# Kernel optimization log

Hardware: AMD Instinct MI355X
Metric: run time of the kernel (lower is better)

The kernel has to match this reference:

```python
import jax, jax.numpy as jnp
import numpy as np

EPS_BN = 1e-5
DIVERSITY_TEMP = 100.0  # lucidrains codebook_diversity_temperature default
COMMIT_W = 1.0
DIVERSITY_W = 1.0
ORTHO_W = 1.0


def conv1d(x, w, b=None, stride=1, pad=0):
    # x: [B,C,T], w: [O,I,K] (torch layout)
    y = jax.lax.conv_general_dilated(x, w, (stride,), [(pad, pad)],
                                     dimension_numbers=('NCH', 'OIH', 'NCH'))
    if b is not None:
        y = y + b[None, :, None]
    return y


def conv1d_transpose(x, w_torch, stride, pad):
    # torch ConvTranspose1d weight: (in, out, k). Equivalent input-dilated conv
    # with flipped kernel and padding k-1-pad.
    w = jnp.flip(jnp.transpose(w_torch, (1, 0, 2)), axis=2)  # -> (out,in,k)
    k = w.shape[2]
    p = k - 1 - pad
    return jax.lax.conv_general_dilated(x, w, (1,), [(p, p)],
                                        lhs_dilation=(stride,),
                                        dimension_numbers=('NCH', 'OIH', 'NCH'))


def batchnorm(x, g, b):
    # training-mode BatchNorm1d: stats over (batch, time) per channel
    m = x.mean(axis=(0, 2), keepdims=True)
    v = x.var(axis=(0, 2), keepdims=True)
    return (x - m) * jax.lax.rsqrt(v + EPS_BN) * g[None, :, None] + b[None, :, None]


def setup_inputs():
    key = jax.random.key(0)
    ks = jax.random.split(key, 10)
    f32 = jnp.float32
    rn = lambda k, shape, s: jax.random.normal(k, shape, f32) * s
    return {
        'x': jax.random.normal(ks[0], (8, 1, 24000), f32),
        # encoder: 1->16->32->64
        'w1': rn(ks[1], (16, 1, 5), 0.3), 'b1': jnp.zeros(16, f32),
        'g1': jnp.ones(16, f32), 'be1': jnp.zeros(16, f32),
        'w2': rn(ks[2], (32, 16, 5), 0.1), 'b2': jnp.zeros(32, f32),
        'g2': jnp.ones(32, f32), 'be2': jnp.zeros(32, f32),
        'w3': rn(ks[3], (64, 32, 25), 0.05), 'b3': jnp.zeros(64, f32),
        'g3': jnp.ones(64, f32), 'be3': jnp.zeros(64, f32),
        # VQ codebook [codebook_size=8192, dim=64]
        'embed': jax.random.normal(ks[4], (8192, 64), f32),
        # decoder
        'dw1': rn(ks[5], (64, 64, 25), 0.05),  # ConvTranspose1d weight (in,out,k)
        'dg1': jnp.ones(64, f32), 'dbe1': jnp.zeros(64, f32),
        'dw2': rn(ks[6], (64, 64, 5), 0.1), 'db2': jnp.zeros(64, f32),
        'dg2': jnp.ones(64, f32), 'dbe2': jnp.zeros(64, f32),
        'dw3': rn(ks[7], (1, 64, 1), 0.2), 'db3': jnp.zeros(1, f32),
        # fixed random subset for orthogonal reg (orthogonal_reg_max_codes=256)
        'ortho_idx': jax.random.randint(ks[8], (256,), 0, 8192),
    }


def reference(x, w1, b1, g1, be1, w2, b2, g2, be2, w3, b3, g3, be3,
              embed, dw1, dg1, dbe1, dw2, db2, dg2, dbe2, dw3, db3, ortho_idx):
    # ---- encoder ----
    h = batchnorm(jax.nn.silu(conv1d(x, w1, b1, 1, 2)), g1, be1)
    h = batchnorm(jax.nn.silu(conv1d(h, w2, b2, 1, 2)), g2, be2)
    z = batchnorm(jnp.tanh(conv1d(h, w3, b3, 12, 12)), g3, be3)  # [B,64,N]
    B, C, N = z.shape
    zf = jnp.transpose(z, (0, 2, 1)).reshape(B * N, C)  # [B*N, 64]

    # ---- VQ: nearest neighbor over codebook ----
    d2 = (jnp.sum(zf * zf, -1, keepdims=True) - 2.0 * (zf @ embed.T)
          + jnp.sum(embed * embed, -1)[None, :])          # [B*N, K]
    dist = jnp.sqrt(jnp.clip(d2, 1e-12))                  # euclidean (cdist p=2)
    idx = jnp.argmin(d2, axis=-1)                         # [B*N]
    q = embed[idx]                                        # codebook gather

    commit = jnp.mean((jax.lax.stop_gradient(q) - zf) ** 2)

    prob = jax.nn.softmax(-dist * DIVERSITY_TEMP, axis=-1)
    avg_prob = prob.mean(axis=0)                          # [K]
    diversity = jnp.sum(avg_prob * jnp.log(jnp.clip(avg_prob, 1e-30)))

    codes = embed[ortho_idx]                              # [256, 64]
    normed = codes * jax.lax.rsqrt(jnp.sum(codes * codes, -1, keepdims=True) + 1e-12)
    cos = normed @ normed.T
    n = codes.shape[0]
    ortho = jnp.sum(cos * cos) / (n * n) - 1.0 / n

    loss = COMMIT_W * commit + DIVERSITY_W * diversity + ORTHO_W * ortho

    # straight-through estimator
    q_st = zf + jax.lax.stop_gradient(q - zf)
    zq = jnp.transpose(q_st.reshape(B, N, C), (0, 2, 1))  # [B,64,N]

    # ---- decoder ----
    d = batchnorm(jax.nn.silu(conv1d_transpose(zq, dw1, 12, 12)), dg1, dbe1)
    d = batchnorm(jax.nn.silu(conv1d(d, dw2, db2, 1, 2)), dg2, dbe2)
    recon = conv1d(d, dw3, db3, 1, 0)

    T = x.shape[2]
    cur = recon.shape[2]
    if cur > T:
        recon = recon[:, :, :T]
    elif cur < T:
        recon = jnp.pad(recon, ((0, 0), (0, 0), (0, T - cur)))
    return recon, idx.reshape(B, N), loss, (commit, diversity, ortho)
```

## Files before the change

### kernel.cpp

```cpp
#include <hip/hip_runtime.h>
#include <math.h>
#include <float.h>

#define DEV __device__ __forceinline__

#define BB 8
#define TT 24000
#define TD 23989
#define NZ 2000
#define ROWS 16000
#define NE 8192
#define NCG 8

typedef __attribute__((ext_vector_type(8))) short bf16x8;
typedef __attribute__((ext_vector_type(4))) float f32x4;

__device__ double g_st[640];
__device__ double g_misc[2];
__device__ float  g_e2[NE];
__device__ float  g_avg[NE];
__device__ float  g_z2[ROWS];
__device__ float  g_rdm[ROWS];
__device__ int    g_rix[ROWS];
__device__ float  g_ob[256 * 64];
__device__ float  g_pmd[ROWS * NCG];
__device__ int    g_pmi[ROWS * NCG];
__device__ int    g_pcc[ROWS * NCG];
__device__ float2 g_cand[ROWS * 256];
__device__ unsigned short g_zbh[ROWS * 64], g_zbl[ROWS * 64];
__device__ unsigned short g_ebh[NE * 64],  g_ebl[NE * 64];
__device__ float  g_s1[16], g_sh1[16];
__device__ float  g_s2[32], g_sh2[32];
__device__ float  g_sd1[64], g_shd1[64];
__device__ float  g_w2f[2560];
__device__ float  g_b2f[32];
__device__ float  g_w3f[64 * 32 * 25];
__device__ float  g_b3f[64];
__device__ float  g_dw2f[64 * 5 * 64];
__device__ float  g_db2f[64];
__device__ float  g_dw1t[64 * 64 * 25];
__device__ float  g_zbn[ROWS * 64];
__device__ double g_zbnd[ROWS * 64];
__device__ float  g_zq[BB * 64 * NZ];
__device__ float  g_y1[BB * 16 * TT];
__device__ float  g_zpre[BB * 64 * NZ];
__device__ float  g_yd1[BB * 64 * TD];
__device__ float  g_y2[BB * 32 * TT];
__device__ float  g_yd2[BB * 64 * TD];

DEV float wsum(float v){
  #pragma unroll
  for (int o = 32; o; o >>= 1) v += __shfl_xor(v, o, 64);
  return v;
}
DEV int clampc(int c){ return c < 0 ? 0 : (c > NE - 1 ? NE - 1 : c); }
DEV float bss(unsigned short s){ union { unsigned u; float f; } v; v.u = ((unsigned)s) << 16; return v.f; }
DEV unsigned short f2bs(float f){
  union { float f; unsigned u; } v; v.f = f;
  unsigned r = (v.u + 0x7FFF + ((v.u >> 16) & 1)) >> 16;
  return (unsigned short)r;
}

__global__ void k_zero(){
  int i = blockIdx.x * 256 + threadIdx.x;
  if (i < 640) g_st[i] = 0.0;
  if (i < 2) g_misc[i] = 0.0;
  if (i < NE) g_avg[i] = 0.f;
}

__global__ void k_embprep(const float* __restrict__ embed){
  int gt = blockIdx.x * 256 + threadIdx.x;
  int gs = gridDim.x * 256;
  for (int i = gt; i < NE * 64; i += gs){
    float v = embed[i];
    unsigned short h = f2bs(v);
    g_ebh[i] = h;
    g_ebl[i] = f2bs(v - bss(h));
  }
  for (int c = gt; c < NE; c += gs){
    float s = 0.f;
    for (int j = 0; j < 64; j++){ float v = embed[c * 64 + j]; s += v * v; }
    g_e2[c] = s;
  }
}

__global__ void k_zsplit(){
  int i = blockIdx.x * 256 + threadIdx.x;
  if (i < ROWS * 64){
    float v = g_zbn[i];
    unsigned short h = f2bs(v);
    g_zbh[i] = h;
    g_zbl[i] = f2bs(v - bss(h));
  }
}

__global__ void k_conv1(const float* __restrict__ x, const float* __restrict__ w1,
                        const float* __restrict__ b1){
  int b = blockIdx.y, t0 = blockIdx.x * 256, tid = threadIdx.x;
  __shared__ float xs[260], wl[80], bl[16], sacc[16], qacc[16];
  if (tid < 80) wl[tid] = w1[tid];
  if (tid < 16){ bl[tid] = b1[tid]; sacc[tid] = 0.f; qacc[tid] = 0.f; }
  for (int i = tid; i < 260; i += 256){ int g = t0 - 2 + i; xs[i] = ((unsigned)g < TT) ? x[b * TT + g] : 0.f; }
  __syncthreads();
  int t = t0 + tid;
  bool ok = t < TT;
  float xv[5];
  #pragma unroll
  for (int k = 0; k < 5; k++) xv[k] = xs[tid + k];
  float out[16];
  #pragma unroll
  for (int c = 0; c < 16; c++){
    float a = bl[c];
    #pragma unroll
    for (int k = 0; k < 5; k++) a += wl[c * 5 + k] * xv[k];
    float o = ok ? a / (1.f + expf(-a)) : 0.f;
    out[c] = o;
    if (ok) g_y1[(b * 16 + c) * TT + t] = o;
  }
  int lane = tid & 63;
  #pragma unroll
  for (int c = 0; c < 16; c++){
    float s = wsum(out[c]);
    float q = wsum(out[c] * out[c]);
    if (lane == 0){ atomicAdd(&sacc[c], s); atomicAdd(&qacc[c], q); }
  }
  __syncthreads();
  if (tid < 16){ atomicAdd(&g_st[tid * 2], (double)sacc[tid]); atomicAdd(&g_st[tid * 2 + 1], (double)qacc[tid]); }
}

__global__ void k_fold2(const float* __restrict__ g1, const float* __restrict__ be1,
                        const float* __restrict__ w2, const float* __restrict__ b2){
  int tid = threadIdx.x;
  if (blockIdx.x == 0 && tid < 16){
    double m = g_st[tid * 2] / 192000.0, v = g_st[tid * 2 + 1] / 192000.0 - m * m;
    float s = g1[tid] / sqrtf((float)v + 1e-5f);
    g_s1[tid] = s; g_sh1[tid] = be1[tid] - (float)m * s;
  }
  if (blockIdx.x == 0 && tid < 32) g_b2f[tid] = b2[tid];
  int gt = blockIdx.x * 256 + tid;
  for (int i = gt; i < 2560; i += 8 * 256){
    int co = i & 31, r = i >> 5, k = r % 5, ci = r / 5;
    g_w2f[i] = w2[(co * 16 + ci) * 5 + k];
  }
}

__global__ void __launch_bounds__(256) k_conv2(){
  int b = blockIdx.y, t0 = blockIdx.x * 256, tid = threadIdx.x;
  __shared__ float xs[16][260];
  __shared__ float sacc[32], qacc[32];
  __shared__ float s1l[16], sh1l[16];
  int lane = tid & 63, wv = tid >> 6;
  int cb = wv * 8;
  if (tid < 32){ sacc[tid] = 0.f; qacc[tid] = 0.f; }
  if (tid < 16){ s1l[tid] = g_s1[tid]; sh1l[tid] = g_sh1[tid]; }
  __syncthreads();
  for (int i = tid; i < 16 * 260; i += 256){
    int ci = i / 260, tt = i - ci * 260, g = t0 - 2 + tt;
    xs[ci][tt] = ((unsigned)g < TT) ? (s1l[ci] * g_y1[(b * 16 + ci) * TT + g] + sh1l[ci]) : 0.f;
  }
  __syncthreads();
  float acc[4][8];
  #pragma unroll
  for (int j = 0; j < 4; j++)
    #pragma unroll
    for (int i = 0; i < 8; i++) acc[j][i] = g_b2f[cb + i];
  for (int ci = 0; ci < 16; ci++){
    #pragma unroll
    for (int k = 0; k < 5; k++){
      const float4* wp = (const float4*)(g_w2f + (ci * 5 + k) * 32 + cb);
      float4 w0 = wp[0], w1v = wp[1];
      float wr[8] = { w0.x, w0.y, w0.z, w0.w, w1v.x, w1v.y, w1v.z, w1v.w };
      #pragma unroll
      for (int j = 0; j < 4; j++){
        float xv = xs[ci][lane + 64 * j + k];
        #pragma unroll
        for (int i = 0; i < 8; i++) acc[j][i] += wr[i] * xv;
      }
    }
  }
  #pragma unroll
  for (int i = 0; i < 8; i++){
    int co = cb + i;
    float s = 0.f, q = 0.f;
    #pragma unroll
    for (int j = 0; j < 4; j++){
      int t = t0 + lane + 64 * j;
      bool ok = t < TT;
      float a = acc[j][i];
      float o = ok ? a / (1.f + expf(-a)) : 0.f;
      if (ok) g_y2[(b * 32 + co) * TT + t] = o;
      s += o; q += o * o;
    }
    s = wsum(s); q = wsum(q);
    if (lane == 0){ atomicAdd(&sacc[co], s); atomicAdd(&qacc[co], q); }
  }
  __syncthreads();
  if (tid < 32){ atomicAdd(&g_st[128 + tid * 2], (double)sacc[tid]); atomicAdd(&g_st[128 + tid * 2 + 1], (double)qacc[tid]); }
}

__global__ void k_fold3(const float* __restrict__ g2, const float* __restrict__ be2,
                        const float* __restrict__ w3, const float* __restrict__ b3){
  int tid = threadIdx.x;
  if (blockIdx.x == 0 && tid < 32){
    double m = g_st[128 + tid * 2] / 192000.0, v = g_st[128 + tid * 2 + 1] / 192000.0 - m * m;
    float s = g2[tid] / sqrtf((float)v + 1e-5f);
    g_s2[tid] = s; g_sh2[tid] = be2[tid] - (float)m * s;
  }
  if (blockIdx.x == 0 && tid >= 64 && tid < 128) g_b3f[tid - 64] = b3[tid - 64];
  int gt = blockIdx.x * 256 + tid;
  for (int i = gt; i < 64 * 32 * 25; i += 64 * 256){
    int co = i & 63, r = i >> 6, k = r % 25, ci = r / 25;
    g_w3f[i] = w3[(co * 32 + ci) * 25 + k];
  }
}

__global__ void __launch_bounds__(256) k_conv3(){
  __shared__ float xs[32][400];
  __shared__ float s2l[32], sh2l[32];
  int tid = threadIdx.x, b = blockIdx.y, t0 = blockIdx.x * 32;
  int lane = tid & 63, wv = tid >> 6;
  int cb = wv * 16;
  int tl = lane & 31, h = lane >> 5;
  if (tid < 32){ s2l[tid] = g_s2[tid]; sh2l[tid] = g_sh2[tid]; }
  __syncthreads();
  int p0 = t0 * 12 - 12;
  for (int i = tid; i < 32 * 397; i += 256){
    int ci = i / 397, pp = i - ci * 397, g = p0 + pp;
    xs[ci][pp] = ((unsigned)g < TT) ? (s2l[ci] * g_y2[(b * 32 + ci) * TT + g] + sh2l[ci]) : 0.f;
  }
  __syncthreads();
  float acc[16];
  #pragma unroll
  for (int i = 0; i < 16; i++) acc[i] = 0.f;
  for (int cii = 0; cii < 16; cii++){
    int ci = h * 16 + cii;
    #pragma unroll
    for (int k = 0; k < 25; k++){
      float xv = xs[ci][tl * 12 + k];
      const float4* wp = (const float4*)(g_w3f + (ci * 25 + k) * 64 + cb);
      float4 a0 = wp[0], a1 = wp[1], a2 = wp[2], a3 = wp[3];
      acc[0] += a0.x * xv; acc[1] += a0.y * xv; acc[2] += a0.z * xv; acc[3] += a0.w * xv;
      acc[4] += a1.x * xv; acc[5] += a1.y * xv; acc[6] += a1.z * xv; acc[7] += a1.w * xv;
      acc[8] += a2.x * xv; acc[9] += a2.y * xv; acc[10] += a2.z * xv; acc[11] += a2.w * xv;
      acc[12] += a3.x * xv; acc[13] += a3.y * xv; acc[14] += a3.z * xv; acc[15] += a3.w * xv;
    }
  }
  #pragma unroll
  for (int i = 0; i < 16; i++) acc[i] += __shfl_xor(acc[i], 32, 64);
  int t = t0 + tl;
  if (h == 0 && t < NZ){
    #pragma unroll
    for (int i = 0; i < 16; i++)
      g_zpre[(b * 64 + cb + i) * NZ + t] = tanhf(acc[i] + g_b3f[cb + i]);
  }
}

__global__ void k_stats(int which, int L, int stoff){
  const float* p = (which == 0) ? g_zpre : (which == 1) ? g_yd1 : g_yd2;
  int co = blockIdx.y, t0 = blockIdx.x * 256, tid = threadIdx.x;
  int t = t0 + tid;
  float s = 0.f, q = 0.f;
  if (t < L){
    for (int b = 0; b < BB; b++){ float v = p[(b * 64 + co) * L + t]; s += v; q += v * v; }
  }
  s = wsum(s); q = wsum(q);
  __shared__ float sa[4], qa[4];
  int w = tid >> 6, lane = tid & 63;
  if (lane == 0){ sa[w] = s; qa[w] = q; }
  __syncthreads();
  if (tid == 0){
    atomicAdd(&g_st[stoff + co * 2], (double)(sa[0] + sa[1] + sa[2] + sa[3]));
    atomicAdd(&g_st[stoff + co * 2 + 1], (double)(qa[0] + qa[1] + qa[2] + qa[3]));
  }
}

__global__ void k_zbn(const float* __restrict__ g3, const float* __restrict__ be3){
  __shared__ float tile[64][65];
  __shared__ float s3[64], sh3[64];
  __shared__ double s3d[64], sh3d[64];
  int tid = threadIdx.x, b = blockIdx.y, n0 = blockIdx.x * 64;
  if (tid < 64){
    double m = g_st[256 + tid * 2] / 16000.0, v = g_st[256 + tid * 2 + 1] / 16000.0 - m * m;
    double sd = (double)g3[tid] / sqrt(v + 1e-5);
    double shd = (double)be3[tid] - m * sd;
    s3d[tid] = sd; sh3d[tid] = shd;
    s3[tid] = (float)sd; sh3[tid] = (float)shd;
  }
  __syncthreads();
  for (int i = tid; i < 64 * 64; i += 256){
    int c = i >> 6, nn = i & 63, n = n0 + nn;
    tile[c][nn] = (n < NZ) ? (s3[c] * g_zpre[(b * 64 + c) * NZ + n] + sh3[c]) : 0.f;
  }
  __syncthreads();
  int lane = tid & 63;
  for (int it = 0; it < 16; ++it){
    int nn = (tid >> 6) + it * 4;
    int n = n0 + nn, c = lane;
    if (n < NZ){
      float v = tile[c][nn];
      int row = b * NZ + n;
      g_zbn[row * 64 + c] = v;
      g_zbnd[row * 64 + c] = s3d[c] * (double)g_zpre[(b * 64 + c) * NZ + n] + sh3d[c];
      float s = wsum(v * v);
      if (lane == 0) g_z2[row] = s;
    }
  }
}

__global__ void __launch_bounds__(256) k_vq1(){
  __shared__ unsigned short bsh[64 * 72];
  __shared__ unsigned short bsl[64 * 72];
  __shared__ float2 ring[64][16];
  __shared__ int cnt[64];
  int tid = threadIdx.x, lane = tid & 63, w = tid >> 6;
  int q = lane >> 4, col = lane & 15;
  int rowbase = blockIdx.x * 64 + w * 16;
  int cbase = blockIdx.y * 1024;
  int grp = blockIdx.y;
  if (tid < 64) cnt[tid] = 0;
  #pragma unroll
  for (int i = 0; i < 4; i++)
    ring[w * 16 + (lane & 15)][(lane >> 4) * 4 + i] = make_float2(FLT_MAX, __int_as_float(NE - 1));
  bf16x8 ah0, ah1, al0, al1;
  {
    const unsigned short* zh = g_zbh + (rowbase + col) * 64;
    const unsigned short* zl = g_zbl + (rowbase + col) * 64;
    ah0 = *(const bf16x8*)(zh + q * 8);
    ah1 = *(const bf16x8*)(zh + 32 + q * 8);
    al0 = *(const bf16x8*)(zl + q * 8);
    al1 = *(const bf16x8*)(zl + 32 + q * 8);
  }
  float z2r[4];
  #pragma unroll
  for (int r = 0; r < 4; r++) z2r[r] = g_z2[rowbase + q * 4 + r];
  float thr[4], lmin[4]; int lamc[4];
  #pragma unroll
  for (int r = 0; r < 4; r++){ thr[r] = FLT_MAX; lmin[r] = FLT_MAX; lamc[r] = NE - 1; }
  float runmin[4] = {FLT_MAX, FLT_MAX, FLT_MAX, FLT_MAX};
  for (int ch = 0; ch < 16; ++ch){
    __syncthreads();
    {
      int cl = tid >> 2, seg = tid & 3;
      int cglob = cbase + ch * 64 + cl;
      *(int4*)&bsh[cl * 72 + seg * 16]     = *(const int4*)(g_ebh + cglob * 64 + seg * 16);
      *(int4*)&bsh[cl * 72 + seg * 16 + 8] = *(const int4*)(g_ebh + cglob * 64 + seg * 16 + 8);
      *(int4*)&bsl[cl * 72 + seg * 16]     = *(const int4*)(g_ebl + cglob * 64 + seg * 16);
      *(int4*)&bsl[cl * 72 + seg * 16 + 8] = *(const int4*)(g_ebl + cglob * 64 + seg * 16 + 8);
    }
    __syncthreads();
    float d2s[4][4];
    float tmin[4] = {FLT_MAX, FLT_MAX, FLT_MAX, FLT_MAX};
    #pragma unroll
    for (int t = 0; t < 4; t++){
      int ct = cbase + ch * 64 + t * 16;
      const unsigned short* bhp = &bsh[(t * 16 + col) * 72];
      const unsigned short* blp = &bsl[(t * 16 + col) * 72];
      bf16x8 bh0 = *(const bf16x8*)(bhp + q * 8);
      bf16x8 bh1 = *(const bf16x8*)(bhp + 32 + q * 8);
      bf16x8 bl0 = *(const bf16x8*)(blp + q * 8);
      bf16x8 bl1 = *(const bf16x8*)(blp + 32 + q * 8);
      f32x4 acc = {0.f, 0.f, 0.f, 0.f};
      acc = __builtin_amdgcn_mfma_f32_16x16x32_bf16(al0, bh0, acc, 0, 0, 0);
      acc = __builtin_amdgcn_mfma_f32_16x16x32_bf16(al1, bh1, acc, 0, 0, 0);
      acc = __builtin_amdgcn_mfma_f32_16x16x32_bf16(ah0, bl0, acc, 0, 0, 0);
      acc = __builtin_amdgcn_mfma_f32_16x16x32_bf16(ah1, bl1, acc, 0, 0, 0);
      acc = __builtin_amdgcn_mfma_f32_16x16x32_bf16(ah0, bh0, acc, 0, 0, 0);
      acc = __builtin_amdgcn_mfma_f32_16x16x32_bf16(ah1, bh1, acc, 0, 0, 0);
      float e2c = g_e2[ct + col];
      #pragma unroll
      for (int r = 0; r < 4; r++){
        float d = z2r[r] + e2c - 2.f * acc[r];
        d2s[t][r] = d;
        if (d < lmin[r]){ lmin[r] = d; lamc[r] = ct + col; }
        tmin[r] = fminf(tmin[r], d);
      }
    }
    #pragma unroll
    for (int r = 0; r < 4; r++){
      float m = tmin[r];
      m = fminf(m, __shfl_xor(m, 1, 64));
      m = fminf(m, __shfl_xor(m, 2, 64));
      m = fminf(m, __shfl_xor(m, 4, 64));
      m = fminf(m, __shfl_xor(m, 8, 64));
      if (m < runmin[r]){
        runmin[r] = m;
        thr[r] = m + 0.71f * sqrtf(fmaxf(m, 0.f)) + 0.13f;
      }
    }
    #pragma unroll
    for (int t = 0; t < 4; t++){
      int ct = cbase + ch * 64 + t * 16;
      bool any = false;
      #pragma unroll
      for (int r = 0; r < 4; r++) if (d2s[t][r] < thr[r]) any = true;
      if (__ballot(any)){
        #pragma unroll
        for (int r = 0; r < 4; r++){
          if (d2s[t][r] < thr[r]){
            int lr = w * 16 + q * 4 + r;
            int s = atomicAdd(&cnt[lr], 1) & 15;
            ring[lr][s] = make_float2(sqrtf(fmaxf(d2s[t][r], 1e-12f)), __int_as_float(ct + col));
          }
        }
      }
    }
  }
  __syncthreads();
  #pragma unroll
  for (int r = 0; r < 4; r++){
    float m = lmin[r]; int c = lamc[r];
    #pragma unroll
    for (int o = 1; o <= 8; o <<= 1){
      float om = __shfl_xor(m, o, 64);
      int oc = __shfl_xor(c, o, 64);
      if (om < m || (om == m && oc < c)){ m = om; c = oc; }
    }
    if (col == 0){
      int gr = rowbase + q * 4 + r;
      g_pmd[gr * NCG + grp] = m;
      g_pmi[gr * NCG + grp] = c;
    }
  }
  if (lane < 16){
    int lr = w * 16 + lane;
    g_pcc[(rowbase + lane) * NCG + grp] = cnt[lr];
  }
  #pragma unroll
  for (int i = 0; i < 4; i++){
    int idx = lane * 4 + i;
    int lr = idx >> 4, s = idx & 15;
    g_cand[(rowbase + lr) * 256 + grp * 16 + s] = ring[w * 16 + lr][s];
  }
}

__global__ void k_vq1b(){
  int row = blockIdx.x * 256 + threadIdx.x;
  if (row >= ROWS) return;
  float best = FLT_MAX; int bi = NE - 1;
  for (int cg = 0; cg < NCG; ++cg){
    float d = g_pmd[row * NCG + cg]; int i = g_pmi[row * NCG + cg];
    if (d < best || (d == best && i < bi)){ best = d; bi = i; }
  }
  g_rdm[row] = sqrtf(fmaxf(best, 1e-12f));
  g_rix[row] = bi;
}

__global__ void __launch_bounds__(256) k_vq3(const float* __restrict__ embed,
                                             float* __restrict__ outIdx){
  __shared__ int   ccode[4][144];
  __shared__ float cdst[4][144];
  __shared__ int   cn[4];
  __shared__ double bsum[4];
  int w = threadIdx.x >> 6, lane = threadIdx.x & 63;
  int row = blockIdx.x * 4 + w;
  float dmin = g_rdm[row];
  int seedc = clampc(g_rix[row]);
  if (lane == 0){ cn[w] = 0; ccode[w][0] = seedc; }
  __syncthreads();
  if (lane == 0) cn[w] = 1;
  int grp = lane & 7;
  int sub = lane >> 3;
  int cnt = g_pcc[row * NCG + grp]; if (cnt > 16) cnt = 16;
  int s0 = sub * 2, s1 = s0 + 2; if (s1 > cnt) s1 = cnt;
  for (int s = s0; s < s1; ++s){
    float2 cd = g_cand[row * 256 + grp * 16 + s];
    float dist = cd.x; int c = clampc(__float_as_int(cd.y));
    if (dist <= dmin + 0.353f && c != seedc){
      int i = atomicAdd(&cn[w], 1);
      ccode[w][i] = c;
    }
  }
  __syncthreads();
  int n = cn[w];
  double zdl = g_zbnd[row * 64 + lane];
  double bd = DBL_MAX; int bc = NE - 1;
  for (int i = 0; i < n; i++){
    int c = ccode[w][i];
    double diff = zdl - (double)embed[c * 64 + lane];
    double d = diff * diff;
    #pragma unroll
    for (int o = 32; o; o >>= 1) d += __shfl_xor(d, o, 64);
    if (lane == 0) cdst[w][i] = (float)d;
    if (d < bd || (d == bd && c < bc)){ bd = d; bc = c; }
  }
  __syncthreads();
  float dminE = (float)sqrt(bd);
  float Zp = 0.f;
  for (int i = lane; i < n; i += 64)
    Zp += expf(-100.f * (sqrtf(cdst[w][i]) - dminE));
  float Z = fmaxf(wsum(Zp), 1e-30f);
  if (lane == 0){
    g_rix[row] = bc;
    outIdx[row] = (float)bc;
    bsum[w] = bd;
  }
  for (int i = lane; i < n; i += 64)
    atomicAdd(&g_avg[ccode[w][i]], expf(-100.f * (sqrtf(cdst[w][i]) - dminE)) / Z);
  __syncthreads();
  if (threadIdx.x == 0)
    atomicAdd(&g_misc[0], bsum[0] + bsum[1] + bsum[2] + bsum[3]);
}

__global__ void k_orthoprep(const float* __restrict__ embed, const int* __restrict__ oidx){
  int tid = threadIdx.x;
  int c = clampc(oidx[tid]);
  float s = 0.f;
  for (int j = 0; j < 64; j++){ float v = embed[c * 64 + j]; s += v * v; }
  float r = 1.f / sqrtf(s + 1e-12f);
  for (int j = 0; j < 64; j++) g_ob[tid * 64 + j] = embed[c * 64 + j] * r;
}

__global__ void k_ortho(){
  int w = threadIdx.x >> 6, lane = threadIdx.x & 63;
  int i = blockIdx.x * 4 + w;
  float acc = 0.f;
  for (int j = lane; j < 256; j += 64){
    float d = 0.f;
    for (int k = 0; k < 64; k++) d += g_ob[i * 64 + k] * g_ob[j * 64 + k];
    acc += d * d;
  }
  acc = wsum(acc);
  if (lane == 0) atomicAdd(&g_misc[1], (double)acc);
}

__global__ void k_div(float* __restrict__ outS){
  int tid = threadIdx.x;
  double part = 0.0;
  for (int c = tid; c < NE; c += 256){
    double p = (double)g_avg[c] / 16000.0;
    double pc = p < 1e-30 ? 1e-30 : p;
    part += p * log(pc);
  }
  __shared__ double red[256];
  red[tid] = part; __syncthreads();
  for (int o = 128; o; o >>= 1){ if (tid < o) red[tid] += red[tid + o]; __syncthreads(); }
  if (tid == 0){
    double diversity = red[0];
    double commit = g_misc[0] / (double)(ROWS * 64);
    double ortho = g_misc[1] / 65536.0 - 1.0 / 256.0;
    double loss = commit + diversity + ortho;
    outS[0] = (float)loss;
    outS[1] = (float)commit;
    outS[2] = (float)diversity;
    outS[3] = (float)ortho;
  }
}

__global__ void k_zq(const float* __restrict__ embed){
  __shared__ float tile[64][65];
  int tid = threadIdx.x, b = blockIdx.y, n0 = blockIdx.x * 64;
  for (int i = tid; i < 64 * 64; i += 256){
    int nn = i >> 6, c = i & 63;
    int n = n0 + nn;
    int code = (n < NZ) ? clampc(g_rix[b * NZ + n]) : 0;
    tile[c][nn] = embed[code * 64 + c];
  }
  __syncthreads();
  for (int i = tid; i < 64 * 64; i += 256){
    int c = i >> 6, nn = i & 63;
    int n = n0 + nn;
    if (n < NZ) g_zq[(b * 64 + c) * NZ + n] = tile[c][nn];
  }
}

__global__ void k_folddw1(const float* __restrict__ dw1){
  int gt = blockIdx.x * 256 + threadIdx.x;
  for (int i = gt; i < 64 * 64 * 25; i += 100 * 256){
    int co = i & 63, r = i >> 6, k = r % 25, ci = r / 25;
    g_dw1t[i] = dw1[(ci * 64 + co) * 25 + (24 - k)];
  }
}

__global__ void __launch_bounds__(256) k_dconv1(){
  __shared__ float xsd[64][68];
  __shared__ float wsh[64 * 25 * 4];
  __shared__ float sacc[4], qacc[4];
  int tid = threadIdx.x, b = blockIdx.y;
  int cb = blockIdx.z * 4;
  int t0 = blockIdx.x * 768;
  int nb = t0 / 12 - 1;
  if (tid < 4){ sacc[tid] = 0.f; qacc[tid] = 0.f; }
  for (int i = tid; i < 64 * 67; i += 256){
    int ci = i / 67, nl = i - ci * 67, n = nb + nl;
    xsd[ci][nl] = ((unsigned)n < NZ) ? g_zq[(b * 64 + ci) * NZ + n] : 0.f;
  }
  for (int i = tid; i < 64 * 25 * 4; i += 256){
    int r = i >> 2, c = i & 3;
    wsh[i] = g_dw1t[r * 64 + cb + c];
  }
  __syncthreads();
  int w = tid >> 6, lane = tid & 63;
  float acc[12];
  #pragma unroll
  for (int p = 0; p < 12; p++) acc[p] = 0.f;
  for (int ci = 0; ci < 64; ci++){
    float xmA = xsd[ci][lane];
    float xm0 = xsd[ci][lane + 1];
    float xmB = xsd[ci][lane + 2];
    const float* wci = wsh + ci * 100 + w;
    acc[0] += wci[0] * xmA;
    acc[0] += wci[12 * 4] * xm0;
    acc[0] += wci[24 * 4] * xmB;
    #pragma unroll
    for (int p = 1; p < 12; p++){
      acc[p] += wci[(12 - p) * 4] * xm0;
      acc[p] += wci[(24 - p) * 4] * xmB;
    }
  }
  bool full = (t0 + 768 <= TD);
  {
    float o[12];
    float s = 0.f, q = 0.f;
    #pragma unroll
    for (int p = 0; p < 12; p++){
      int t = t0 + lane * 12 + p;
      float a = acc[p];
      float v = (t < TD) ? a / (1.f + expf(-a)) : 0.f;
      o[p] = v; s += v; q += v * v;
    }
    float* dst = &g_yd1[(b * 64 + cb + w) * TD + t0 + lane * 12];
    if (full){
      ((float4*)dst)[0] = make_float4(o[0], o[1], o[2], o[3]);
      ((float4*)dst)[1] = make_float4(o[4], o[5], o[6], o[7]);
      ((float4*)dst)[2] = make_float4(o[8], o[9], o[10], o[11]);
    } else {
      #pragma unroll
      for (int p = 0; p < 12; p++){
        int t = t0 + lane * 12 + p;
        if (t < TD) dst[p] = o[p];
      }
    }
    s = wsum(s); q = wsum(q);
    if (lane == 0){ atomicAdd(&sacc[w], s); atomicAdd(&qacc[w], q); }
  }
  __syncthreads();
  if (tid < 4){
    atomicAdd(&g_st[384 + (cb + tid) * 2], (double)sacc[tid]);
    atomicAdd(&g_st[384 + (cb + tid) * 2 + 1], (double)qacc[tid]);
  }
}

__global__ void k_foldd2(const float* __restrict__ dg1, const float* __restrict__ dbe1,
                         const float* __restrict__ dw2, const float* __restrict__ db2){
  int tid = threadIdx.x;
  if (blockIdx.x == 0 && tid < 64){
    double m = g_st[384 + tid * 2] / 191912.0, v = g_st[384 + tid * 2 + 1] / 191912.0 - m * m;
    float sc = dg1[tid] / sqrtf((float)v + 1e-5f);
    g_sd1[tid] = sc; g_shd1[tid] = dbe1[tid] - (float)m * sc;
    g_db2f[tid] = db2[tid];
  }
  int gt = blockIdx.x * 256 + tid;
  for (int i = gt; i < 64 * 5 * 64; i += 32 * 256){
    int co = i & 63, r = i >> 6, k = r % 5, ci = r / 5;
    g_dw2f[i] = dw2[(co * 64 + ci) * 5 + k];
  }
}

__global__ void __launch_bounds__(256) k_dconv2(){
  __shared__ float xs[32][388];
  __shared__ float sdl[64], shdl[64];
  __shared__ float sacc[64], qacc[64];
  int tid = threadIdx.x, b = blockIdx.y, t0 = blockIdx.x * 384;
  int lane = tid & 63, wv = tid >> 6;
  int cb = wv * 16;
  if (tid < 64){ sdl[tid] = g_sd1[tid]; shdl[tid] = g_shd1[tid]; sacc[tid] = 0.f; qacc[tid] = 0.f; }
  float acc[6][16];
  #pragma unroll
  for (int j = 0; j < 6; j++)
    #pragma unroll
    for (int i = 0; i < 16; i++) acc[j][i] = g_db2f[cb + i];
  for (int half = 0; half < 2; ++half){
    __syncthreads();
    for (int i = tid; i < 32 * 388; i += 256){
      int ci = i / 388, tt = i - ci * 388, g = t0 - 2 + tt;
      int cia = half * 32 + ci;
      xs[ci][tt] = ((unsigned)g < TD) ? (sdl[cia] * g_yd1[(b * 64 + cia) * TD + g] + shdl[cia]) : 0.f;
    }
    __syncthreads();
    for (int ci = 0; ci < 32; ci++){
      int cia = half * 32 + ci;
      #pragma unroll
      for (int k = 0; k < 5; k++){
        const float4* wp = (const float4*)(g_dw2f + (cia * 5 + k) * 64 + cb);
        float4 w0 = wp[0], w1 = wp[1], w2v = wp[2], w3v = wp[3];
        float wr[16] = { w0.x, w0.y, w0.z, w0.w, w1.x, w1.y, w1.z, w1.w,
                         w2v.x, w2v.y, w2v.z, w2v.w, w3v.x, w3v.y, w3v.z, w3v.w };
        #pragma unroll
        for (int j = 0; j < 6; j++){
          float xv = xs[ci][lane + 64 * j + k];
          #pragma unroll
          for (int i = 0; i < 16; i++) acc[j][i] += wr[i] * xv;
        }
      }
    }
  }
  #pragma unroll
  for (int i = 0; i < 16; i++){
    int co = cb + i;
    float s = 0.f, q = 0.f;
    #pragma unroll
    for (int j = 0; j < 6; j++){
      int t = t0 + lane + 64 * j;
      bool ok = t < TD;
      float a = acc[j][i];
      float o = ok ? a / (1.f + expf(-a)) : 0.f;
      if (ok) g_yd2[(b * 64 + co) * TD + t] = o;
      s += o; q += o * o;
    }
    s = wsum(s); q = wsum(q);
    if (lane == 0){ atomicAdd(&sacc[co], s); atomicAdd(&qacc[co], q); }
  }
  __syncthreads();
  if (tid < 64){
    atomicAdd(&g_st[512 + tid * 2], (double)sacc[tid]);
    atomicAdd(&g_st[512 + tid * 2 + 1], (double)qacc[tid]);
  }
}

__global__ void k_recon(const float* __restrict__ dg2, const float* __restrict__ dbe2,
                        const float* __restrict__ dw3, const float* __restrict__ db3,
                        float* __restrict__ outR){
  __shared__ float wf[64];
  __shared__ float bsh2;
  int tid = threadIdx.x, b = blockIdx.y, t0 = blockIdx.x * 256;
  if (tid < 64){
    double m = g_st[512 + tid * 2] / 191912.0, v = g_st[512 + tid * 2 + 1] / 191912.0 - m * m;
    float sc = dg2[tid] / sqrtf((float)v + 1e-5f);
    float shv = dbe2[tid] - (float)m * sc;
    wf[tid] = dw3[tid] * sc;
    float contrib = wsum(dw3[tid] * shv);
    if (tid == 0) bsh2 = db3[0] + contrib;
  }
  __syncthreads();
  int t = t0 + tid;
  if (t < TT){
    if (t < TD){
      float a = bsh2;
      for (int ci = 0; ci < 64; ci++) a += wf[ci] * g_yd2[(b * 64 + ci) * TD + t];
      outR[b * TT + t] = a;
    } else {
      outR[b * TT + t] = 0.f;
    }
  }
}

extern "C" void kernel_launch(void* const* d_in, const int* in_sizes, int n_in,
                              void* d_out, int out_size, void* d_ws, size_t ws_size,
                              hipStream_t stream){
  (void)in_sizes; (void)n_in; (void)out_size; (void)d_ws; (void)ws_size;
  const float* x    = (const float*)d_in[0];
  const float* w1   = (const float*)d_in[1];
  const float* b1   = (const float*)d_in[2];
  const float* g1   = (const float*)d_in[3];
  const float* be1  = (const float*)d_in[4];
  const float* w2   = (const float*)d_in[5];
  const float* b2   = (const float*)d_in[6];
  const float* g2   = (const float*)d_in[7];
  const float* be2  = (const float*)d_in[8];
  const float* w3   = (const float*)d_in[9];
  const float* b3   = (const float*)d_in[10];
  const float* g3   = (const float*)d_in[11];
  const float* be3  = (const float*)d_in[12];
  const float* embed= (const float*)d_in[13];
  const float* dw1  = (const float*)d_in[14];
  const float* dg1  = (const float*)d_in[15];
  const float* dbe1 = (const float*)d_in[16];
  const float* dw2  = (const float*)d_in[17];
  const float* db2  = (const float*)d_in[18];
  const float* dg2  = (const float*)d_in[19];
  const float* dbe2 = (const float*)d_in[20];
  const float* dw3  = (const float*)d_in[21];
  const float* db3  = (const float*)d_in[22];
  const int* oidx   = (const int*)d_in[23];

  float* out    = (float*)d_out;
  float* outIdx = out + 192000;
  float* outS   = out + 208000;

  hipLaunchKernelGGL(k_zero, dim3(32), dim3(256), 0, stream);
  hipLaunchKernelGGL(k_embprep, dim3(64), dim3(256), 0, stream, embed);
  hipLaunchKernelGGL(k_conv1, dim3(94, 8), dim3(256), 0, stream, x, w1, b1);
  hipLaunchKernelGGL(k_fold2, dim3(8), dim3(256), 0, stream, g1, be1, w2, b2);
  hipLaunchKernelGGL(k_conv2, dim3(94, 8), dim3(256), 0, stream);
  hipLaunchKernelGGL(k_fold3, dim3(64), dim3(256), 0, stream, g2, be2, w3, b3);
  hipLaunchKernelGGL(k_conv3, dim3(63, 8), dim3(256), 0, stream);
  hipLaunchKernelGGL(k_stats, dim3(8, 64), dim3(256), 0, stream, 0, NZ, 256);
  hipLaunchKernelGGL(k_zbn, dim3(32, 8), dim3(256), 0, stream, g3, be3);
  hipLaunchKernelGGL(k_zsplit, dim3(4000), dim3(256), 0, stream);
  hipLaunchKernelGGL(k_vq1, dim3(250, 8), dim3(256), 0, stream);
  hipLaunchKernelGGL(k_vq1b, dim3(63), dim3(256), 0, stream);
  hipLaunchKernelGGL(k_vq3, dim3(4000), dim3(256), 0, stream, embed, outIdx);
  hipLaunchKernelGGL(k_orthoprep, dim3(1), dim3(256), 0, stream, embed, oidx);
  hipLaunchKernelGGL(k_ortho, dim3(64), dim3(256), 0, stream);
  hipLaunchKernelGGL(k_div, dim3(1), dim3(256), 0, stream, outS);
  hipLaunchKernelGGL(k_zq, dim3(32, 8), dim3(256), 0, stream, embed);
  hipLaunchKernelGGL(k_folddw1, dim3(100), dim3(256), 0, stream, dw1);
  hipLaunchKernelGGL(k_dconv1, dim3(32, 8, 16), dim3(256), 0, stream);
  hipLaunchKernelGGL(k_foldd2, dim3(32), dim3(256), 0, stream, dg1, dbe1, dw2, db2);
  hipLaunchKernelGGL(k_dconv2, dim3(63, 8), dim3(256), 0, stream);
  hipLaunchKernelGGL(k_recon, dim3(94, 8), dim3(256), 0, stream, dg2, dbe2, dw3, db3, out);
}
```

Measured before the change: 892.4 us.

## Register-block transposed conv over four input positions per thread

Each thread of the decoder transposed-conv kernel now computes 48 outputs (4 input positions × 12 phases) instead of 12. Weights are held in registers and loaded as float4 from a per-channel layout, and inputs are staged in 16-channel chunks. This spreads each weight load across more FMAs and cuts shared-memory traffic, at the cost of more registers, a grid reduced to 1024 blocks, and extra block barriers per chunk.

```diff
diff --git a/kernel.cpp b/kernel.cpp
--- a/kernel.cpp
+++ b/kernel.cpp
@@ -571,68 +571,86 @@
   }
 }
 
-__global__ void __launch_bounds__(256) k_dconv1(){
-  __shared__ float xsd[64][68];
-  __shared__ float wsh[64 * 25 * 4];
+__global__ void __launch_bounds__(256, 3) k_dconv1(){
+  __shared__ float xsd[16][260];
+  __shared__ float wsh[4][64][28];
   __shared__ float sacc[4], qacc[4];
   int tid = threadIdx.x, b = blockIdx.y;
   int cb = blockIdx.z * 4;
-  int t0 = blockIdx.x * 768;
-  int nb = t0 / 12 - 1;
+  int t0 = blockIdx.x * 3072;
+  int nb = blockIdx.x * 256 - 1;
+  int w = tid >> 6, lane = tid & 63;
   if (tid < 4){ sacc[tid] = 0.f; qacc[tid] = 0.f; }
-  for (int i = tid; i < 64 * 67; i += 256){
-    int ci = i / 67, nl = i - ci * 67, n = nb + nl;
-    xsd[ci][nl] = ((unsigned)n < NZ) ? g_zq[(b * 64 + ci) * NZ + n] : 0.f;
-  }
-  for (int i = tid; i < 64 * 25 * 4; i += 256){
-    int r = i >> 2, c = i & 3;
-    wsh[i] = g_dw1t[r * 64 + cb + c];
-  }
-  __syncthreads();
-  int w = tid >> 6, lane = tid & 63;
-  float acc[12];
-  #pragma unroll
-  for (int p = 0; p < 12; p++) acc[p] = 0.f;
-  for (int ci = 0; ci < 64; ci++){
-    float xmA = xsd[ci][lane];
-    float xm0 = xsd[ci][lane + 1];
-    float xmB = xsd[ci][lane + 2];
-    const float* wci = wsh + ci * 100 + w;
-    acc[0] += wci[0] * xmA;
-    acc[0] += wci[12 * 4] * xm0;
-    acc[0] += wci[24 * 4] * xmB;
-    #pragma unroll
-    for (int p = 1; p < 12; p++){
-      acc[p] += wci[(12 - p) * 4] * xm0;
-      acc[p] += wci[(24 - p) * 4] * xmB;
-    }
-  }
-  bool full = (t0 + 768 <= TD);
-  {
+  for (int i = tid; i < 6400; i += 256){
+    int c = i & 3, r = i >> 2;
+    int k = r % 25, ci = r / 25;
+    wsh[c][ci][k] = g_dw1t[r * 64 + cb + c];
+  }
+  float acc[4][12];
+  #pragma unroll
+  for (int q = 0; q < 4; q++)
+    #pragma unroll
+    for (int p = 0; p < 12; p++) acc[q][p] = 0.f;
+  for (int cc = 0; cc < 4; ++cc){
+    __syncthreads();
+    for (int i = tid; i < 16 * 259; i += 256){
+      int ci = i / 259, nl = i - ci * 259;
+      int n = nb + nl;
+      xsd[ci][nl] = ((unsigned)n < NZ) ? g_zq[(b * 64 + cc * 16 + ci) * NZ + n] : 0.f;
+    }
+    __syncthreads();
+    #pragma unroll 2
+    for (int ci = 0; ci < 16; ++ci){
+      int cia = cc * 16 + ci;
+      const float4* xp = (const float4*)&xsd[ci][4 * lane];
+      float4 xA = xp[0], xB = xp[1];
+      float xv[6] = { xA.x, xA.y, xA.z, xA.w, xB.x, xB.y };
+      const float4* wp = (const float4*)&wsh[w][cia][0];
+      float4 w0 = wp[0], w1 = wp[1], w2 = wp[2], w3 = wp[3], w4 = wp[4], w5 = wp[5];
+      float wv[25] = { w0.x, w0.y, w0.z, w0.w, w1.x, w1.y, w1.z, w1.w,
+                       w2.x, w2.y, w2.z, w2.w, w3.x, w3.y, w3.z, w3.w,
+                       w4.x, w4.y, w4.z, w4.w, w5.x, w5.y, w5.z, w5.w,
+                       wsh[w][cia][24] };
+      #pragma unroll
+      for (int q = 0; q < 4; ++q){
+        acc[q][0] += wv[0] * xv[q];
+        acc[q][0] += wv[12] * xv[q + 1];
+        acc[q][0] += wv[24] * xv[q + 2];
+        #pragma unroll
+        for (int p = 1; p < 12; ++p){
+          acc[q][p] += wv[12 - p] * xv[q + 1];
+          acc[q][p] += wv[24 - p] * xv[q + 2];
+        }
+      }
+    }
+  }
+  bool full = (t0 + 3072 <= TD);
+  float s = 0.f, qs = 0.f;
+  float* dst = &g_yd1[(b * 64 + cb + w) * TD + t0 + lane * 48];
+  #pragma unroll
+  for (int q = 0; q < 4; ++q){
     float o[12];
-    float s = 0.f, q = 0.f;
-    #pragma unroll
-    for (int p = 0; p < 12; p++){
-      int t = t0 + lane * 12 + p;
-      float a = acc[p];
+    #pragma unroll
+    for (int p = 0; p < 12; ++p){
+      int t = t0 + lane * 48 + q * 12 + p;
+      float a = acc[q][p];
       float v = (t < TD) ? a / (1.f + expf(-a)) : 0.f;
-      o[p] = v; s += v; q += v * v;
-    }
-    float* dst = &g_yd1[(b * 64 + cb + w) * TD + t0 + lane * 12];
+      o[p] = v; s += v; qs += v * v;
+    }
     if (full){
-      ((float4*)dst)[0] = make_float4(o[0], o[1], o[2], o[3]);
-      ((float4*)dst)[1] = make_float4(o[4], o[5], o[6], o[7]);
-      ((float4*)dst)[2] = make_float4(o[8], o[9], o[10], o[11]);
+      ((float4*)(dst + q * 12))[0] = make_float4(o[0], o[1], o[2], o[3]);
+      ((float4*)(dst + q * 12))[1] = make_float4(o[4], o[5], o[6], o[7]);
+      ((float4*)(dst + q * 12))[2] = make_float4(o[8], o[9], o[10], o[11]);
     } else {
       #pragma unroll
-      for (int p = 0; p < 12; p++){
-        int t = t0 + lane * 12 + p;
-        if (t < TD) dst[p] = o[p];
+      for (int p = 0; p < 12; ++p){
+        int t = t0 + lane * 48 + q * 12 + p;
+        if (t < TD) dst[q * 12 + p] = o[p];
       }
     }
-    s = wsum(s); q = wsum(q);
-    if (lane == 0){ atomicAdd(&sacc[w], s); atomicAdd(&qacc[w], q); }
-  }
+  }
+  s = wsum(s); qs = wsum(qs);
+  if (lane == 0){ atomicAdd(&sacc[w], s); atomicAdd(&qacc[w], qs); }
   __syncthreads();
   if (tid < 4){
     atomicAdd(&g_st[384 + (cb + tid) * 2], (double)sacc[tid]);
@@ -795,7 +813,7 @@
   hipLaunchKernelGGL(k_div, dim3(1), dim3(256), 0, stream, outS);
   hipLaunchKernelGGL(k_zq, dim3(32, 8), dim3(256), 0, stream, embed);
   hipLaunchKernelGGL(k_folddw1, dim3(100), dim3(256), 0, stream, dw1);
-  hipLaunchKernelGGL(k_dconv1, dim3(32, 8, 16), dim3(256), 0, stream);
+  hipLaunchKernelGGL(k_dconv1, dim3(8, 8, 16), dim3(256), 0, stream);
   hipLaunchKernelGGL(k_foldd2, dim3(32), dim3(256), 0, stream, dg1, dbe1, dw2, db2);
   hipLaunchKernelGGL(k_dconv2, dim3(63, 8), dim3(256), 0, stream);
   hipLaunchKernelGGL(k_recon, dim3(94, 8), dim3(256), 0, stream, dg2, dbe2, dw3, db3, out);
```

New measurement: 973.7 us. 9.1% more time.
